# Optimization experiments

Hardware: AMD Instinct MI355X
Metric: run time of the kernel (lower is better)

Reference implementation:

```python
import jax, jax.numpy as jnp
import numpy as np

EMBED_DIM = 1024
NUM_HEADS = 16
B, L = 4, 2048


def setup_inputs() -> dict:
    key = jax.random.key(0)
    ks = jax.random.split(key, 5)
    scale = 0.02
    return {
        "x": jax.random.normal(ks[0], (B, L, EMBED_DIM), dtype=jnp.float32),
        "Wqkv_w": jax.random.normal(ks[1], (3 * EMBED_DIM, EMBED_DIM), dtype=jnp.float32) * scale,
        "Wqkv_b": jax.random.normal(ks[2], (3 * EMBED_DIM,), dtype=jnp.float32) * scale,
        "out_w": jax.random.normal(ks[3], (EMBED_DIM, EMBED_DIM), dtype=jnp.float32) * scale,
        "out_b": jax.random.normal(ks[4], (EMBED_DIM,), dtype=jnp.float32) * scale,
    }


def reference(x, Wqkv_w, Wqkv_b, out_w, out_b):
    Bb, Ll, D = x.shape
    H = NUM_HEADS
    hd = D // H
    # fused QKV projection (torch Linear: x @ W.T + b)
    qkv = jnp.einsum("bld,ed->ble", x, Wqkv_w) + Wqkv_b  # [B, L, 3D]
    q, k, v = jnp.split(qkv, 3, axis=-1)
    # [B, H, L, hd]
    q = q.reshape(Bb, Ll, H, hd).transpose(0, 2, 1, 3)
    k = k.reshape(Bb, Ll, H, hd).transpose(0, 2, 1, 3)
    v = v.reshape(Bb, Ll, H, hd).transpose(0, 2, 1, 3)
    scale = 1.0 / jnp.sqrt(jnp.asarray(hd, dtype=x.dtype))
    scores = jnp.einsum("bhqd,bhkd->bhqk", q, k) * scale  # [B, H, L, L]
    # causal mask (upper triangle above diagonal masked)
    causal = jnp.tril(jnp.ones((Ll, Ll), dtype=bool))
    scores = jnp.where(causal, scores, jnp.asarray(-jnp.inf, dtype=scores.dtype))
    attn = jax.nn.softmax(scores, axis=-1)
    attn_out = jnp.einsum("bhqk,bhkd->bhqd", attn, v)  # [B, H, L, hd]
    attn_out = attn_out.transpose(0, 2, 1, 3).reshape(Bb, Ll, D)
    out = jnp.einsum("bld,ed->ble", attn_out, out_w) + out_b
    return out
```

## Files before the change

kernel.cpp:

```cpp
#include <hip/hip_runtime.h>
#include <stdint.h>

#define DEV __device__ __forceinline__

typedef unsigned short u16;
typedef __bf16 bf16x8 __attribute__((ext_vector_type(8)));
typedef float f32x4 __attribute__((ext_vector_type(4)));
typedef u16 u16x8 __attribute__((ext_vector_type(8)));

#define MFMA_BF16(A, B, C) __builtin_amdgcn_mfma_f32_16x16x32_bf16(A, B, C, 0, 0, 0)
#define EXP2(x) __builtin_amdgcn_exp2f(x)

DEV u16 f2bf(float f) {
    unsigned x;
    __builtin_memcpy(&x, &f, 4);
    unsigned r = (x + 0x7fffu + ((x >> 16) & 1u)) >> 16;
    return (u16)r;
}

DEV u16 f2bf_fast(float f) {
    unsigned x;
    __builtin_memcpy(&x, &f, 4);
    return (u16)((x + 0x8000u) >> 16);
}

DEV void storeC(u16* p, float v) { *p = f2bf(v); }
DEV void storeC(float* p, float v) { *p = v; }

DEV void async_copy16(const u16* g, u16* l) {
    __builtin_amdgcn_global_load_lds(
        (__attribute__((address_space(1))) unsigned int*)g,
        (__attribute__((address_space(3))) unsigned int*)l, 16, 0, 0);
}

constexpr int N_X = 8192 * 1024, N_WQ = 3072 * 1024, N_WO = 1024 * 1024;

__global__ __launch_bounds__(256)
void cvt_all(const float* __restrict__ x, const float* __restrict__ wq,
             const float* __restrict__ wo, u16* __restrict__ out) {
    const int i = (blockIdx.x * 256 + threadIdx.x) * 4;
    const float* src;
    if (i < N_X) src = x + i;
    else if (i < N_X + N_WQ) src = wq + (i - N_X);
    else src = wo + (i - N_X - N_WQ);
    const float4 v = *(const float4*)src;
    ushort4 o;
    o.x = f2bf(v.x);
    o.y = f2bf(v.y);
    o.z = f2bf(v.z);
    o.w = f2bf(v.w);
    *(ushort4*)(out + i) = o;
}

template <typename OT, bool VSPLIT>
__global__ __launch_bounds__(256, 2)
void gemm_bt_bias(const u16* __restrict__ A, const u16* __restrict__ Bw,
                  const float* __restrict__ bias, OT* __restrict__ C,
                  u16* __restrict__ vT, int M, int N, int K) {
    __shared__ __attribute__((aligned(16))) u16 sA[2][128 * 32];
    __shared__ __attribute__((aligned(16))) u16 sB[2][128 * 32];

    const int tid  = threadIdx.x;
    const int lane = tid & 63;
    const int wave = tid >> 6;
    const int m0 = blockIdx.x * 128;
    const int n0 = blockIdx.y * 128;
    const int wm = (wave & 1) * 64;
    const int wn = (wave >> 1) * 64;
    const int fr = lane & 15;
    const int q4 = lane >> 4;

    const int r0 = tid >> 2;
    const int c0 = (tid & 3) * 8;
    const u16* gA0 = A + (size_t)(m0 + r0) * K + c0;
    const u16* gA1 = A + (size_t)(m0 + 64 + r0) * K + c0;
    const u16* gB0 = Bw + (size_t)(n0 + r0) * K + c0;
    const u16* gB1 = Bw + (size_t)(n0 + 64 + r0) * K + c0;

    f32x4 acc[4][4];
#pragma unroll
    for (int i = 0; i < 4; i++)
#pragma unroll
        for (int j = 0; j < 4; j++) acc[i][j] = (f32x4){0.f, 0.f, 0.f, 0.f};

    for (int k0 = 0; k0 < K; k0 += 64) {
#pragma unroll
        for (int p = 0; p < 2; ++p) {
            async_copy16(gA0 + k0 + p * 32, &sA[p][tid * 8]);
            async_copy16(gA1 + k0 + p * 32, &sA[p][2048 + tid * 8]);
            async_copy16(gB0 + k0 + p * 32, &sB[p][tid * 8]);
            async_copy16(gB1 + k0 + p * 32, &sB[p][2048 + tid * 8]);
        }
        __syncthreads();

#pragma unroll
        for (int p = 0; p < 2; ++p) {
            bf16x8 af[4], bfr[4];
#pragma unroll
            for (int i = 0; i < 4; i++)
                af[i] = *(const bf16x8*)&sA[p][(wm + i * 16 + fr) * 32 + q4 * 8];
#pragma unroll
            for (int j = 0; j < 4; j++)
                bfr[j] = *(const bf16x8*)&sB[p][(wn + j * 16 + fr) * 32 + q4 * 8];
#pragma unroll
            for (int i = 0; i < 4; i++)
#pragma unroll
                for (int j = 0; j < 4; j++)
                    acc[i][j] = MFMA_BF16(af[i], bfr[j], acc[i][j]);
        }
        __syncthreads();
    }

#pragma unroll
    for (int j = 0; j < 4; j++) {
        const int col = n0 + wn + j * 16 + fr;
        const float bv = bias[col];
        if (VSPLIT && col >= 2048) {
#pragma unroll
            for (int i = 0; i < 4; i++) {
                const int row = m0 + wm + i * 16 + q4 * 4;
                ushort4 o;
                o.x = f2bf(acc[i][j][0] + bv);
                o.y = f2bf(acc[i][j][1] + bv);
                o.z = f2bf(acc[i][j][2] + bv);
                o.w = f2bf(acc[i][j][3] + bv);
                *(ushort4*)&vT[(size_t)(col - 2048) * 8192 + row] = o;
            }
        } else {
#pragma unroll
            for (int i = 0; i < 4; i++) {
                const int row = m0 + wm + i * 16 + q4 * 4;
#pragma unroll
                for (int r = 0; r < 4; r++)
                    storeC(&C[(size_t)(row + r) * N + col], acc[i][j][r] + bv);
            }
        }
    }
}

constexpr int Lc = 2048, Dc = 1024;

__global__ __launch_bounds__(256, 4)
void attn_fa(const u16* __restrict__ qkv, const u16* __restrict__ vT,
             u16* __restrict__ outb) {
    __shared__ __attribute__((aligned(16))) u16 sK[64 * 72];
    __shared__ __attribute__((aligned(16))) u16 sVT[64 * 72];
    __shared__ __attribute__((aligned(16))) u16 sP[4][2][16 * 72];

    const int tid  = threadIdx.x;
    const int lane = tid & 63;
    const int wave = tid >> 6;
    const int fr = lane & 15;
    const int q4 = lane >> 4;

    const int id = blockIdx.x;
    const int g  = (id & 7) + 8 * (id >> 7);
    const int bx = (id >> 3) & 15;
    const int h = g & 15;
    const int b = g >> 4;
    const int qblkA = bx;
    const int qblkB = 31 - bx;

    constexpr float CEXP = 0.18033688011112042f;

    const int qrowA = qblkA * 64 + wave * 16 + fr;
    const int qrowB = qblkB * 64 + wave * 16 + fr;
    const u16* qptrA = qkv + ((size_t)(b * Lc + qrowA) * 3) * Dc + h * 64;
    const u16* qptrB = qkv + ((size_t)(b * Lc + qrowB) * 3) * Dc + h * 64;
    bf16x8 qfA[2], qfB[2];
    qfA[0] = *(const bf16x8*)(qptrA + q4 * 8);
    qfA[1] = *(const bf16x8*)(qptrA + 32 + q4 * 8);
    qfB[0] = *(const bf16x8*)(qptrB + q4 * 8);
    qfB[1] = *(const bf16x8*)(qptrB + 32 + q4 * 8);

    f32x4 oA[4], oB[4];
#pragma unroll
    for (int t = 0; t < 4; t++) {
        oA[t] = (f32x4){0.f, 0.f, 0.f, 0.f};
        oB[t] = (f32x4){0.f, 0.f, 0.f, 0.f};
    }
    float mA = -3.4e38f, lA = 0.f, mB = -3.4e38f, lB = 0.f;

    const int q_local = wave * 16 + fr;

    const int rr = tid >> 3;
    const int oo = tid & 7;
    const u16* kg = qkv + ((size_t)(b * Lc) * 3 + 1) * Dc + h * 64 + oo * 8;
    const u16* vg = vT + (size_t)(h * 64) * 8192 + b * Lc + oo * 8;

    u16x8 kr[2], vr[2];
#pragma unroll
    for (int c = 0; c < 2; ++c) {
        kr[c] = *(const u16x8*)(kg + (size_t)(c * 32 + rr) * 3072);
        vr[c] = *(const u16x8*)(vg + (size_t)(c * 32 + rr) * 8192);
    }

    u16* sPA = &sP[wave][0][0];
    u16* sPB = &sP[wave][1][0];

    for (int jb = 0; jb <= qblkB; ++jb) {
        __syncthreads();
#pragma unroll
        for (int c = 0; c < 2; ++c) {
            *(u16x8*)&sK[(c * 32 + rr) * 72 + oo * 8] = kr[c];
            *(u16x8*)&sVT[(c * 32 + rr) * 72 + oo * 8] = vr[c];
        }
        __syncthreads();
        if (jb < qblkB) {
#pragma unroll
            for (int c = 0; c < 2; ++c) {
                kr[c] = *(const u16x8*)(kg + (size_t)((jb + 1) * 64 + c * 32 + rr) * 3072);
                vr[c] = *(const u16x8*)(vg + (size_t)(c * 32 + rr) * 8192 + (jb + 1) * 64);
            }
        }

        const bool doA = (jb <= qblkA);

        f32x4 sA_[4], sB_[4];
#pragma unroll
        for (int t = 0; t < 4; t++) {
            const bf16x8 kf0 = *(const bf16x8*)&sK[(t * 16 + fr) * 72 + q4 * 8];
            const bf16x8 kf1 = *(const bf16x8*)&sK[(t * 16 + fr) * 72 + 32 + q4 * 8];
            sB_[t] = (f32x4){0.f, 0.f, 0.f, 0.f};
            sB_[t] = MFMA_BF16(kf0, qfB[0], sB_[t]);
            sB_[t] = MFMA_BF16(kf1, qfB[1], sB_[t]);
            if (doA) {
                sA_[t] = (f32x4){0.f, 0.f, 0.f, 0.f};
                sA_[t] = MFMA_BF16(kf0, qfA[0], sA_[t]);
                sA_[t] = MFMA_BF16(kf1, qfA[1], sA_[t]);
            }
        }

        {
            if (jb == qblkB) {
#pragma unroll
                for (int t = 0; t < 4; t++)
#pragma unroll
                    for (int r = 0; r < 4; r++)
                        if (t * 16 + q4 * 4 + r > q_local) sB_[t][r] = -1e30f;
            }
            float mx = sB_[0][0];
#pragma unroll
            for (int t = 0; t < 4; t++)
#pragma unroll
                for (int r = 0; r < 4; r++) mx = fmaxf(mx, sB_[t][r]);
            mx = fmaxf(mx, __shfl_xor(mx, 16));
            mx = fmaxf(mx, __shfl_xor(mx, 32));
            const float mnew = fmaxf(mB, mx);
            const float alpha = EXP2((mB - mnew) * CEXP);
            float sum = 0.f;
#pragma unroll
            for (int t = 0; t < 4; t++) {
#pragma unroll
                for (int r = 0; r < 4; r++) {
                    const float p = EXP2((sB_[t][r] - mnew) * CEXP);
                    sB_[t][r] = p;
                    sum += p;
                }
                ushort4 o;
                o.x = f2bf_fast(sB_[t][0]);
                o.y = f2bf_fast(sB_[t][1]);
                o.z = f2bf_fast(sB_[t][2]);
                o.w = f2bf_fast(sB_[t][3]);
                *(ushort4*)&sPB[fr * 72 + t * 16 + q4 * 4] = o;
            }
            sum += __shfl_xor(sum, 16);
            sum += __shfl_xor(sum, 32);
            lB = alpha * lB + sum;
            mB = mnew;
#pragma unroll
            for (int t = 0; t < 4; t++)
#pragma unroll
                for (int r = 0; r < 4; r++) oB[t][r] *= alpha;
        }

        if (doA) {
            if (jb == qblkA) {
#pragma unroll
                for (int t = 0; t < 4; t++)
#pragma unroll
                    for (int r = 0; r < 4; r++)
                        if (t * 16 + q4 * 4 + r > q_local) sA_[t][r] = -1e30f;
            }
            float mx = sA_[0][0];
#pragma unroll
            for (int t = 0; t < 4; t++)
#pragma unroll
                for (int r = 0; r < 4; r++) mx = fmaxf(mx, sA_[t][r]);
            mx = fmaxf(mx, __shfl_xor(mx, 16));
            mx = fmaxf(mx, __shfl_xor(mx, 32));
            const float mnew = fmaxf(mA, mx);
            const float alpha = EXP2((mA - mnew) * CEXP);
            float sum = 0.f;
#pragma unroll
            for (int t = 0; t < 4; t++) {
#pragma unroll
                for (int r = 0; r < 4; r++) {
                    const float p = EXP2((sA_[t][r] - mnew) * CEXP);
                    sA_[t][r] = p;
                    sum += p;
                }
                ushort4 o;
                o.x = f2bf_fast(sA_[t][0]);
                o.y = f2bf_fast(sA_[t][1]);
                o.z = f2bf_fast(sA_[t][2]);
                o.w = f2bf_fast(sA_[t][3]);
                *(ushort4*)&sPA[fr * 72 + t * 16 + q4 * 4] = o;
            }
            sum += __shfl_xor(sum, 16);
            sum += __shfl_xor(sum, 32);
            lA = alpha * lA + sum;
            mA = mnew;
#pragma unroll
            for (int t = 0; t < 4; t++)
#pragma unroll
                for (int r = 0; r < 4; r++) oA[t][r] *= alpha;
        }

#pragma unroll
        for (int ks = 0; ks < 2; ++ks) {
            const bf16x8 pfB = *(const bf16x8*)&sPB[fr * 72 + ks * 32 + q4 * 8];
            bf16x8 pfA;
            if (doA) pfA = *(const bf16x8*)&sPA[fr * 72 + ks * 32 + q4 * 8];
#pragma unroll
            for (int t = 0; t < 4; t++) {
                const bf16x8 vf = *(const bf16x8*)&sVT[(t * 16 + fr) * 72 + ks * 32 + q4 * 8];
                oB[t] = MFMA_BF16(vf, pfB, oB[t]);
                if (doA) oA[t] = MFMA_BF16(vf, pfA, oA[t]);
            }
        }
    }

    const float rlA = 1.0f / lA;
    const float rlB = 1.0f / lB;
    u16* orowA = outb + (size_t)(b * Lc + qblkA * 64 + wave * 16 + fr) * Dc + h * 64;
    u16* orowB = outb + (size_t)(b * Lc + qblkB * 64 + wave * 16 + fr) * Dc + h * 64;
#pragma unroll
    for (int t = 0; t < 4; t++) {
        ushort4 a, o;
        a.x = f2bf(oA[t][0] * rlA);
        a.y = f2bf(oA[t][1] * rlA);
        a.z = f2bf(oA[t][2] * rlA);
        a.w = f2bf(oA[t][3] * rlA);
        *(ushort4*)(orowA + t * 16 + q4 * 4) = a;
        o.x = f2bf(oB[t][0] * rlB);
        o.y = f2bf(oB[t][1] * rlB);
        o.z = f2bf(oB[t][2] * rlB);
        o.w = f2bf(oB[t][3] * rlB);
        *(ushort4*)(orowB + t * 16 + q4 * 4) = o;
    }
}

extern "C" void kernel_launch(void* const* d_in, const int* in_sizes, int n_in,
                              void* d_out, int out_size, void* d_ws, size_t ws_size,
                              hipStream_t stream) {
    const float* x    = (const float*)d_in[0];
    const float* wqkv = (const float*)d_in[1];
    const float* bqkv = (const float*)d_in[2];
    const float* wout = (const float*)d_in[3];
    const float* bout = (const float*)d_in[4];
    float* out = (float*)d_out;

    u16* qkv    = (u16*)d_ws;
    u16* attn   = qkv + (size_t)8192 * 3072;
    u16* xbf    = attn + (size_t)8192 * 1024;
    u16* wqkvbf = xbf + (size_t)8192 * 1024;
    u16* woutbf = wqkvbf + (size_t)3072 * 1024;
    u16* vT     = woutbf + (size_t)1024 * 1024;

    dim3 blk(256);
    cvt_all<<<(N_X + N_WQ + N_WO) / 1024, blk, 0, stream>>>(x, wqkv, wout, xbf);

    gemm_bt_bias<u16, true><<<dim3(8192 / 128, 3072 / 128), blk, 0, stream>>>(
        xbf, wqkvbf, bqkv, qkv, vT, 8192, 3072, 1024);
    attn_fa<<<dim3(1024), blk, 0, stream>>>(qkv, vT, attn);
    gemm_bt_bias<float, false><<<dim3(8192 / 128, 1024 / 128), blk, 0, stream>>>(
        attn, woutbf, bout, out, nullptr, 8192, 1024, 1024);
}
```

Measured before the change: 267.1 us.

## Rewrite GEMMs with 8-wave 256x128 tiles, triple-buffered LDS, and swizzled layout

Replaces the 4-wave 128x128 double-sync GEMM with a 512-thread kernel computing 256x128 tiles using a 3-stage LDS ring of 64-wide K slices, XOR-swizzled shared memory, and prefetch loads interleaved between two MFMA phases with s_setprio. Also remaps block IDs across XCDs for L2 locality. The aim is to hide global-load latency behind MFMA work and cut LDS bank conflicts. In exchange it uses far more LDS per block (144KB), which limits occupancy, and adds more barriers per K step.

```diff
diff --git a/kernel.cpp b/kernel.cpp
--- a/kernel.cpp
+++ b/kernel.cpp
@@ -31,6 +31,12 @@
     __builtin_amdgcn_global_load_lds(
         (__attribute__((address_space(1))) unsigned int*)g,
         (__attribute__((address_space(3))) unsigned int*)l, 16, 0, 0);
+}
+
+DEV void wg_barrier() {
+    asm volatile("" ::: "memory");
+    __builtin_amdgcn_s_barrier();
+    asm volatile("" ::: "memory");
 }
 
 constexpr int N_X = 8192 * 1024, N_WQ = 3072 * 1024, N_WO = 1024 * 1024;
@@ -53,29 +59,33 @@
 }
 
 template <typename OT, bool VSPLIT>
-__global__ __launch_bounds__(256, 2)
-void gemm_bt_bias(const u16* __restrict__ A, const u16* __restrict__ Bw,
-                  const float* __restrict__ bias, OT* __restrict__ C,
-                  u16* __restrict__ vT, int M, int N, int K) {
-    __shared__ __attribute__((aligned(16))) u16 sA[2][128 * 32];
-    __shared__ __attribute__((aligned(16))) u16 sB[2][128 * 32];
+__global__ __launch_bounds__(512, 2)
+void gemm_8ph(const u16* __restrict__ A, const u16* __restrict__ Bw,
+              const float* __restrict__ bias, OT* __restrict__ C,
+              u16* __restrict__ vT, int M, int N, int K, int ntn) {
+    __shared__ __attribute__((aligned(16))) u16 sA[3][256 * 64];
+    __shared__ __attribute__((aligned(16))) u16 sB[3][128 * 64];
 
     const int tid  = threadIdx.x;
     const int lane = tid & 63;
     const int wave = tid >> 6;
-    const int m0 = blockIdx.x * 128;
-    const int n0 = blockIdx.y * 128;
-    const int wm = (wave & 1) * 64;
-    const int wn = (wave >> 1) * 64;
     const int fr = lane & 15;
     const int q4 = lane >> 4;
-
-    const int r0 = tid >> 2;
-    const int c0 = (tid & 3) * 8;
-    const u16* gA0 = A + (size_t)(m0 + r0) * K + c0;
-    const u16* gA1 = A + (size_t)(m0 + 64 + r0) * K + c0;
-    const u16* gB0 = Bw + (size_t)(n0 + r0) * K + c0;
-    const u16* gB1 = Bw + (size_t)(n0 + 64 + r0) * K + c0;
+    const int wr = wave >> 1;
+    const int wc = wave & 1;
+
+    const int cpx = gridDim.x >> 3;
+    const int wg = (blockIdx.x & 7) * cpx + (blockIdx.x >> 3);
+    const int mt = wg / ntn, nt = wg % ntn;
+    const int m0 = mt * 256, n0 = nt * 128;
+
+    const int crow = tid >> 3;
+    const int ccol = ((tid & 7) ^ (crow & 7)) * 8;
+    const u16* pA = A + (size_t)(m0 + crow) * K + ccol;
+    const u16* pB = Bw + (size_t)(n0 + crow) * K + ccol;
+    const size_t rK = (size_t)64 * K;
+
+    const int NT = K >> 6;
 
     f32x4 acc[4][4];
 #pragma unroll
@@ -83,42 +93,99 @@
 #pragma unroll
         for (int j = 0; j < 4; j++) acc[i][j] = (f32x4){0.f, 0.f, 0.f, 0.f};
 
-    for (int k0 = 0; k0 < K; k0 += 64) {
-#pragma unroll
-        for (int p = 0; p < 2; ++p) {
-            async_copy16(gA0 + k0 + p * 32, &sA[p][tid * 8]);
-            async_copy16(gA1 + k0 + p * 32, &sA[p][2048 + tid * 8]);
-            async_copy16(gB0 + k0 + p * 32, &sB[p][tid * 8]);
-            async_copy16(gB1 + k0 + p * 32, &sB[p][2048 + tid * 8]);
-        }
-        __syncthreads();
-
-#pragma unroll
-        for (int p = 0; p < 2; ++p) {
-            bf16x8 af[4], bfr[4];
-#pragma unroll
-            for (int i = 0; i < 4; i++)
-                af[i] = *(const bf16x8*)&sA[p][(wm + i * 16 + fr) * 32 + q4 * 8];
-#pragma unroll
-            for (int j = 0; j < 4; j++)
-                bfr[j] = *(const bf16x8*)&sB[p][(wn + j * 16 + fr) * 32 + q4 * 8];
-#pragma unroll
-            for (int i = 0; i < 4; i++)
-#pragma unroll
-                for (int j = 0; j < 4; j++)
-                    acc[i][j] = MFMA_BF16(af[i], bfr[j], acc[i][j]);
-        }
-        __syncthreads();
+#pragma unroll
+    for (int p = 0; p < 4; p++) async_copy16(pA + p * rK, &sA[0][p * 4096 + tid * 8]);
+#pragma unroll
+    for (int p = 0; p < 2; p++) async_copy16(pB + p * rK, &sB[0][p * 4096 + tid * 8]);
+#pragma unroll
+    for (int p = 0; p < 4; p++) async_copy16(pA + p * rK + 64, &sA[1][p * 4096 + tid * 8]);
+#pragma unroll
+    for (int p = 0; p < 2; p++) async_copy16(pB + p * rK + 64, &sB[1][p * 4096 + tid * 8]);
+    asm volatile("s_waitcnt vmcnt(6)" ::: "memory");
+    wg_barrier();
+
+    int sl = 0;
+    for (int t = 0; t < NT; ++t) {
+        const u16* bufA = sA[sl];
+        const u16* bufB = sB[sl];
+        const int s2 = (sl >= 1) ? sl - 1 : 2;
+        const bool st = (t + 2 < NT);
+        const int ko = (t + 2) * 64;
+
+        bf16x8 af[4][2], bf[4][2];
+
+#pragma unroll
+        for (int i = 0; i < 4; i++) {
+            const int row = wr * 64 + i * 16 + fr;
+#pragma unroll
+            for (int kk = 0; kk < 2; kk++)
+                af[i][kk] = *(const bf16x8*)
+                    &bufA[row * 64 + (((kk * 64 + q4 * 16) ^ ((row & 7) << 4)) >> 1)];
+        }
+#pragma unroll
+        for (int j = 0; j < 2; j++) {
+            const int row = wc * 64 + j * 16 + fr;
+#pragma unroll
+            for (int kk = 0; kk < 2; kk++)
+                bf[j][kk] = *(const bf16x8*)
+                    &bufB[row * 64 + (((kk * 64 + q4 * 16) ^ ((row & 7) << 4)) >> 1)];
+        }
+        if (st) {
+#pragma unroll
+            for (int p = 0; p < 3; p++)
+                async_copy16(pA + p * rK + ko, &sA[s2][p * 4096 + tid * 8]);
+        }
+        wg_barrier();
+        __builtin_amdgcn_s_setprio(1);
+#pragma unroll
+        for (int i = 0; i < 4; i++)
+#pragma unroll
+            for (int j = 0; j < 2; j++) {
+                acc[i][j] = MFMA_BF16(af[i][0], bf[j][0], acc[i][j]);
+                acc[i][j] = MFMA_BF16(af[i][1], bf[j][1], acc[i][j]);
+            }
+        __builtin_amdgcn_s_setprio(0);
+        wg_barrier();
+
+#pragma unroll
+        for (int j = 2; j < 4; j++) {
+            const int row = wc * 64 + j * 16 + fr;
+#pragma unroll
+            for (int kk = 0; kk < 2; kk++)
+                bf[j][kk] = *(const bf16x8*)
+                    &bufB[row * 64 + (((kk * 64 + q4 * 16) ^ ((row & 7) << 4)) >> 1)];
+        }
+        if (st) {
+            async_copy16(pA + 3 * rK + ko, &sA[s2][3 * 4096 + tid * 8]);
+#pragma unroll
+            for (int p = 0; p < 2; p++)
+                async_copy16(pB + p * rK + ko, &sB[s2][p * 4096 + tid * 8]);
+        }
+        if (t < NT - 2) asm volatile("s_waitcnt vmcnt(6)" ::: "memory");
+        else            asm volatile("s_waitcnt vmcnt(0)" ::: "memory");
+        wg_barrier();
+        __builtin_amdgcn_s_setprio(1);
+#pragma unroll
+        for (int i = 0; i < 4; i++)
+#pragma unroll
+            for (int j = 2; j < 4; j++) {
+                acc[i][j] = MFMA_BF16(af[i][0], bf[j][0], acc[i][j]);
+                acc[i][j] = MFMA_BF16(af[i][1], bf[j][1], acc[i][j]);
+            }
+        __builtin_amdgcn_s_setprio(0);
+        wg_barrier();
+
+        sl = (sl < 2) ? sl + 1 : 0;
     }
 
 #pragma unroll
     for (int j = 0; j < 4; j++) {
-        const int col = n0 + wn + j * 16 + fr;
+        const int col = n0 + wc * 64 + j * 16 + fr;
         const float bv = bias[col];
         if (VSPLIT && col >= 2048) {
 #pragma unroll
             for (int i = 0; i < 4; i++) {
-                const int row = m0 + wm + i * 16 + q4 * 4;
+                const int row = m0 + wr * 64 + i * 16 + q4 * 4;
                 ushort4 o;
                 o.x = f2bf(acc[i][j][0] + bv);
                 o.y = f2bf(acc[i][j][1] + bv);
@@ -129,7 +196,7 @@
         } else {
 #pragma unroll
             for (int i = 0; i < 4; i++) {
-                const int row = m0 + wm + i * 16 + q4 * 4;
+                const int row = m0 + wr * 64 + i * 16 + q4 * 4;
 #pragma unroll
                 for (int r = 0; r < 4; r++)
                     storeC(&C[(size_t)(row + r) * N + col], acc[i][j][r] + bv);
@@ -368,12 +435,11 @@
     u16* woutbf = wqkvbf + (size_t)3072 * 1024;
     u16* vT     = woutbf + (size_t)1024 * 1024;
 
-    dim3 blk(256);
-    cvt_all<<<(N_X + N_WQ + N_WO) / 1024, blk, 0, stream>>>(x, wqkv, wout, xbf);
-
-    gemm_bt_bias<u16, true><<<dim3(8192 / 128, 3072 / 128), blk, 0, stream>>>(
-        xbf, wqkvbf, bqkv, qkv, vT, 8192, 3072, 1024);
-    attn_fa<<<dim3(1024), blk, 0, stream>>>(qkv, vT, attn);
-    gemm_bt_bias<float, false><<<dim3(8192 / 128, 1024 / 128), blk, 0, stream>>>(
-        attn, woutbf, bout, out, nullptr, 8192, 1024, 1024);
-}
+    cvt_all<<<(N_X + N_WQ + N_WO) / 1024, dim3(256), 0, stream>>>(x, wqkv, wout, xbf);
+
+    gemm_8ph<u16, true><<<dim3(768), dim3(512), 0, stream>>>(
+        xbf, wqkvbf, bqkv, qkv, vT, 8192, 3072, 1024, 24);
+    attn_fa<<<dim3(1024), dim3(256), 0, stream>>>(qkv, vT, attn);
+    gemm_8ph<float, false><<<dim3(256), dim3(512), 0, stream>>>(
+        attn, woutbf, bout, out, nullptr, 8192, 1024, 1024, 8);
+}
```

Result: no change. 267.9 us (+0.3%).

## Process four query blocks per attention workgroup to reuse K/V tiles

Applied to the files above, without the earlier changes.

Each attention workgroup now handles four causally balanced query blocks (bx, 15-bx, 16+bx, 31-bx) instead of two, so every K/V tile staged in shared memory serves up to four query blocks. The grid is halved to 512 workgroups and launch bounds drop to 2 waves-per-EU to make room for the larger register state (four O accumulators and four Q fragments). This reduces global K/V loads and barrier count per unit of work, but it lowers occupancy and parallelism: with 512 workgroups on a 256-CU part there may be under-filled CUs and less latency hiding.

```diff
diff --git a/kernel.cpp b/kernel.cpp
--- a/kernel.cpp
+++ b/kernel.cpp
@@ -140,12 +140,12 @@
 
 constexpr int Lc = 2048, Dc = 1024;
 
-__global__ __launch_bounds__(256, 4)
+__global__ __launch_bounds__(256, 2)
 void attn_fa(const u16* __restrict__ qkv, const u16* __restrict__ vT,
              u16* __restrict__ outb) {
     __shared__ __attribute__((aligned(16))) u16 sK[64 * 72];
     __shared__ __attribute__((aligned(16))) u16 sVT[64 * 72];
-    __shared__ __attribute__((aligned(16))) u16 sP[4][2][16 * 72];
+    __shared__ __attribute__((aligned(16))) u16 sP[4][4][16 * 72];
 
     const int tid  = threadIdx.x;
     const int lane = tid & 63;
@@ -154,32 +154,35 @@
     const int q4 = lane >> 4;
 
     const int id = blockIdx.x;
-    const int g  = (id & 7) + 8 * (id >> 7);
-    const int bx = (id >> 3) & 15;
+    const int g  = (id & 7) + 8 * (id >> 6);
+    const int bx = (id >> 3) & 7;
     const int h = g & 15;
     const int b = g >> 4;
-    const int qblkA = bx;
-    const int qblkB = 31 - bx;
+    const int qA = bx, qB = 15 - bx, qC = 16 + bx, qD = 31 - bx;
 
     constexpr float CEXP = 0.18033688011112042f;
 
-    const int qrowA = qblkA * 64 + wave * 16 + fr;
-    const int qrowB = qblkB * 64 + wave * 16 + fr;
-    const u16* qptrA = qkv + ((size_t)(b * Lc + qrowA) * 3) * Dc + h * 64;
-    const u16* qptrB = qkv + ((size_t)(b * Lc + qrowB) * 3) * Dc + h * 64;
-    bf16x8 qfA[2], qfB[2];
-    qfA[0] = *(const bf16x8*)(qptrA + q4 * 8);
-    qfA[1] = *(const bf16x8*)(qptrA + 32 + q4 * 8);
-    qfB[0] = *(const bf16x8*)(qptrB + q4 * 8);
-    qfB[1] = *(const bf16x8*)(qptrB + 32 + q4 * 8);
-
-    f32x4 oA[4], oB[4];
+    bf16x8 qfA[2], qfB[2], qfC[2], qfD[2];
+#define LOADQ(qf, qblk)                                                     \
+    {                                                                       \
+        const int qrow = (qblk) * 64 + wave * 16 + fr;                      \
+        const u16* qp = qkv + ((size_t)(b * Lc + qrow) * 3) * Dc + h * 64;  \
+        qf[0] = *(const bf16x8*)(qp + q4 * 8);                              \
+        qf[1] = *(const bf16x8*)(qp + 32 + q4 * 8);                         \
+    }
+    LOADQ(qfA, qA) LOADQ(qfB, qB) LOADQ(qfC, qC) LOADQ(qfD, qD)
+#undef LOADQ
+
+    f32x4 oA[4], oB[4], oC[4], oD[4];
 #pragma unroll
     for (int t = 0; t < 4; t++) {
         oA[t] = (f32x4){0.f, 0.f, 0.f, 0.f};
         oB[t] = (f32x4){0.f, 0.f, 0.f, 0.f};
+        oC[t] = (f32x4){0.f, 0.f, 0.f, 0.f};
+        oD[t] = (f32x4){0.f, 0.f, 0.f, 0.f};
     }
     float mA = -3.4e38f, lA = 0.f, mB = -3.4e38f, lB = 0.f;
+    float mC = -3.4e38f, lC = 0.f, mD = -3.4e38f, lD = 0.f;
 
     const int q_local = wave * 16 + fr;
 
@@ -197,8 +200,48 @@
 
     u16* sPA = &sP[wave][0][0];
     u16* sPB = &sP[wave][1][0];
-
-    for (int jb = 0; jb <= qblkB; ++jb) {
+    u16* sPC = &sP[wave][2][0];
+    u16* sPD = &sP[wave][3][0];
+
+#define SM_TILE(S, mS, lS, oS, sPp, qblk)                                   \
+    {                                                                       \
+        if (jb == (qblk)) {                                                 \
+            _Pragma("unroll") for (int t = 0; t < 4; t++)                   \
+                _Pragma("unroll") for (int r = 0; r < 4; r++)               \
+                    if (t * 16 + q4 * 4 + r > q_local) S[t][r] = -1e30f;    \
+        }                                                                   \
+        float mx = S[0][0];                                                 \
+        _Pragma("unroll") for (int t = 0; t < 4; t++)                       \
+            _Pragma("unroll") for (int r = 0; r < 4; r++)                   \
+                mx = fmaxf(mx, S[t][r]);                                    \
+        mx = fmaxf(mx, __shfl_xor(mx, 16));                                 \
+        mx = fmaxf(mx, __shfl_xor(mx, 32));                                 \
+        const float mnew = fmaxf(mS, mx);                                   \
+        const float alpha = EXP2((mS - mnew) * CEXP);                       \
+        float sum = 0.f;                                                    \
+        _Pragma("unroll") for (int t = 0; t < 4; t++) {                     \
+            _Pragma("unroll") for (int r = 0; r < 4; r++) {                 \
+                const float p = EXP2((S[t][r] - mnew) * CEXP);              \
+                S[t][r] = p;                                                \
+                sum += p;                                                   \
+            }                                                               \
+            ushort4 o;                                                      \
+            o.x = f2bf_fast(S[t][0]);                                       \
+            o.y = f2bf_fast(S[t][1]);                                       \
+            o.z = f2bf_fast(S[t][2]);                                       \
+            o.w = f2bf_fast(S[t][3]);                                       \
+            *(ushort4*)&sPp[fr * 72 + t * 16 + q4 * 4] = o;                 \
+        }                                                                   \
+        sum += __shfl_xor(sum, 16);                                         \
+        sum += __shfl_xor(sum, 32);                                         \
+        lS = alpha * lS + sum;                                              \
+        mS = mnew;                                                          \
+        _Pragma("unroll") for (int t = 0; t < 4; t++)                       \
+            _Pragma("unroll") for (int r = 0; r < 4; r++)                   \
+                oS[t][r] *= alpha;                                          \
+    }
+
+    for (int jb = 0; jb <= qD; ++jb) {
         __syncthreads();
 #pragma unroll
         for (int c = 0; c < 2; ++c) {
@@ -206,7 +249,7 @@
             *(u16x8*)&sVT[(c * 32 + rr) * 72 + oo * 8] = vr[c];
         }
         __syncthreads();
-        if (jb < qblkB) {
+        if (jb < qD) {
 #pragma unroll
             for (int c = 0; c < 2; ++c) {
                 kr[c] = *(const u16x8*)(kg + (size_t)((jb + 1) * 64 + c * 32 + rr) * 3072);
@@ -214,16 +257,28 @@
             }
         }
 
-        const bool doA = (jb <= qblkA);
-
-        f32x4 sA_[4], sB_[4];
+        const bool doA = (jb <= qA);
+        const bool doB = (jb <= qB);
+        const bool doC = (jb <= qC);
+
+        f32x4 sA_[4], sB_[4], sC_[4], sD_[4];
 #pragma unroll
         for (int t = 0; t < 4; t++) {
             const bf16x8 kf0 = *(const bf16x8*)&sK[(t * 16 + fr) * 72 + q4 * 8];
             const bf16x8 kf1 = *(const bf16x8*)&sK[(t * 16 + fr) * 72 + 32 + q4 * 8];
-            sB_[t] = (f32x4){0.f, 0.f, 0.f, 0.f};
-            sB_[t] = MFMA_BF16(kf0, qfB[0], sB_[t]);
-            sB_[t] = MFMA_BF16(kf1, qfB[1], sB_[t]);
+            sD_[t] = (f32x4){0.f, 0.f, 0.f, 0.f};
+            sD_[t] = MFMA_BF16(kf0, qfD[0], sD_[t]);
+            sD_[t] = MFMA_BF16(kf1, qfD[1], sD_[t]);
+            if (doC) {
+                sC_[t] = (f32x4){0.f, 0.f, 0.f, 0.f};
+                sC_[t] = MFMA_BF16(kf0, qfC[0], sC_[t]);
+                sC_[t] = MFMA_BF16(kf1, qfC[1], sC_[t]);
+            }
+            if (doB) {
+                sB_[t] = (f32x4){0.f, 0.f, 0.f, 0.f};
+                sB_[t] = MFMA_BF16(kf0, qfB[0], sB_[t]);
+                sB_[t] = MFMA_BF16(kf1, qfB[1], sB_[t]);
+            }
             if (doA) {
                 sA_[t] = (f32x4){0.f, 0.f, 0.f, 0.f};
                 sA_[t] = MFMA_BF16(kf0, qfA[0], sA_[t]);
@@ -231,124 +286,49 @@
             }
         }
 
-        {
-            if (jb == qblkB) {
-#pragma unroll
-                for (int t = 0; t < 4; t++)
-#pragma unroll
-                    for (int r = 0; r < 4; r++)
-                        if (t * 16 + q4 * 4 + r > q_local) sB_[t][r] = -1e30f;
-            }
-            float mx = sB_[0][0];
-#pragma unroll
-            for (int t = 0; t < 4; t++)
-#pragma unroll
-                for (int r = 0; r < 4; r++) mx = fmaxf(mx, sB_[t][r]);
-            mx = fmaxf(mx, __shfl_xor(mx, 16));
-            mx = fmaxf(mx, __shfl_xor(mx, 32));
-            const float mnew = fmaxf(mB, mx);
-            const float alpha = EXP2((mB - mnew) * CEXP);
-            float sum = 0.f;
-#pragma unroll
-            for (int t = 0; t < 4; t++) {
-#pragma unroll
-                for (int r = 0; r < 4; r++) {
-                    const float p = EXP2((sB_[t][r] - mnew) * CEXP);
-                    sB_[t][r] = p;
-                    sum += p;
-                }
-                ushort4 o;
-                o.x = f2bf_fast(sB_[t][0]);
-                o.y = f2bf_fast(sB_[t][1]);
-                o.z = f2bf_fast(sB_[t][2]);
-                o.w = f2bf_fast(sB_[t][3]);
-                *(ushort4*)&sPB[fr * 72 + t * 16 + q4 * 4] = o;
-            }
-            sum += __shfl_xor(sum, 16);
-            sum += __shfl_xor(sum, 32);
-            lB = alpha * lB + sum;
-            mB = mnew;
-#pragma unroll
-            for (int t = 0; t < 4; t++)
-#pragma unroll
-                for (int r = 0; r < 4; r++) oB[t][r] *= alpha;
-        }
-
-        if (doA) {
-            if (jb == qblkA) {
-#pragma unroll
-                for (int t = 0; t < 4; t++)
-#pragma unroll
-                    for (int r = 0; r < 4; r++)
-                        if (t * 16 + q4 * 4 + r > q_local) sA_[t][r] = -1e30f;
-            }
-            float mx = sA_[0][0];
-#pragma unroll
-            for (int t = 0; t < 4; t++)
-#pragma unroll
-                for (int r = 0; r < 4; r++) mx = fmaxf(mx, sA_[t][r]);
-            mx = fmaxf(mx, __shfl_xor(mx, 16));
-            mx = fmaxf(mx, __shfl_xor(mx, 32));
-            const float mnew = fmaxf(mA, mx);
-            const float alpha = EXP2((mA - mnew) * CEXP);
-            float sum = 0.f;
-#pragma unroll
-            for (int t = 0; t < 4; t++) {
-#pragma unroll
-                for (int r = 0; r < 4; r++) {
-                    const float p = EXP2((sA_[t][r] - mnew) * CEXP);
-                    sA_[t][r] = p;
-                    sum += p;
-                }
-                ushort4 o;
-                o.x = f2bf_fast(sA_[t][0]);
-                o.y = f2bf_fast(sA_[t][1]);
-                o.z = f2bf_fast(sA_[t][2]);
-                o.w = f2bf_fast(sA_[t][3]);
-                *(ushort4*)&sPA[fr * 72 + t * 16 + q4 * 4] = o;
-            }
-            sum += __shfl_xor(sum, 16);
-            sum += __shfl_xor(sum, 32);
-            lA = alpha * lA + sum;
-            mA = mnew;
-#pragma unroll
-            for (int t = 0; t < 4; t++)
-#pragma unroll
-                for (int r = 0; r < 4; r++) oA[t][r] *= alpha;
-        }
+        SM_TILE(sD_, mD, lD, oD, sPD, qD);
+        if (doC) SM_TILE(sC_, mC, lC, oC, sPC, qC);
+        if (doB) SM_TILE(sB_, mB, lB, oB, sPB, qB);
+        if (doA) SM_TILE(sA_, mA, lA, oA, sPA, qA);
 
 #pragma unroll
         for (int ks = 0; ks < 2; ++ks) {
-            const bf16x8 pfB = *(const bf16x8*)&sPB[fr * 72 + ks * 32 + q4 * 8];
-            bf16x8 pfA;
+            const bf16x8 pfD = *(const bf16x8*)&sPD[fr * 72 + ks * 32 + q4 * 8];
+            bf16x8 pfC, pfB, pfA;
+            if (doC) pfC = *(const bf16x8*)&sPC[fr * 72 + ks * 32 + q4 * 8];
+            if (doB) pfB = *(const bf16x8*)&sPB[fr * 72 + ks * 32 + q4 * 8];
             if (doA) pfA = *(const bf16x8*)&sPA[fr * 72 + ks * 32 + q4 * 8];
 #pragma unroll
             for (int t = 0; t < 4; t++) {
                 const bf16x8 vf = *(const bf16x8*)&sVT[(t * 16 + fr) * 72 + ks * 32 + q4 * 8];
-                oB[t] = MFMA_BF16(vf, pfB, oB[t]);
+                oD[t] = MFMA_BF16(vf, pfD, oD[t]);
+                if (doC) oC[t] = MFMA_BF16(vf, pfC, oC[t]);
+                if (doB) oB[t] = MFMA_BF16(vf, pfB, oB[t]);
                 if (doA) oA[t] = MFMA_BF16(vf, pfA, oA[t]);
             }
         }
     }
-
-    const float rlA = 1.0f / lA;
-    const float rlB = 1.0f / lB;
-    u16* orowA = outb + (size_t)(b * Lc + qblkA * 64 + wave * 16 + fr) * Dc + h * 64;
-    u16* orowB = outb + (size_t)(b * Lc + qblkB * 64 + wave * 16 + fr) * Dc + h * 64;
-#pragma unroll
-    for (int t = 0; t < 4; t++) {
-        ushort4 a, o;
-        a.x = f2bf(oA[t][0] * rlA);
-        a.y = f2bf(oA[t][1] * rlA);
-        a.z = f2bf(oA[t][2] * rlA);
-        a.w = f2bf(oA[t][3] * rlA);
-        *(ushort4*)(orowA + t * 16 + q4 * 4) = a;
-        o.x = f2bf(oB[t][0] * rlB);
-        o.y = f2bf(oB[t][1] * rlB);
-        o.z = f2bf(oB[t][2] * rlB);
-        o.w = f2bf(oB[t][3] * rlB);
-        *(ushort4*)(orowB + t * 16 + q4 * 4) = o;
-    }
+#undef SM_TILE
+
+#define WR_OUT(oS, lS, qblk)                                                      \
+    {                                                                             \
+        const float rl = 1.0f / lS;                                               \
+        u16* orow =                                                               \
+            outb + (size_t)(b * Lc + (qblk) * 64 + wave * 16 + fr) * Dc + h * 64; \
+        _Pragma("unroll") for (int t = 0; t < 4; t++) {                           \
+            ushort4 o;                                                            \
+            o.x = f2bf(oS[t][0] * rl);                                            \
+            o.y = f2bf(oS[t][1] * rl);                                            \
+            o.z = f2bf(oS[t][2] * rl);                                            \
+            o.w = f2bf(oS[t][3] * rl);                                            \
+            *(ushort4*)(orow + t * 16 + q4 * 4) = o;                              \
+        }                                                                         \
+    }
+    WR_OUT(oA, lA, qA)
+    WR_OUT(oB, lB, qB)
+    WR_OUT(oC, lC, qC)
+    WR_OUT(oD, lD, qD)
+#undef WR_OUT
 }
 
 extern "C" void kernel_launch(void* const* d_in, const int* in_sizes, int n_in,
@@ -373,7 +353,7 @@
 
     gemm_bt_bias<u16, true><<<dim3(8192 / 128, 3072 / 128), blk, 0, stream>>>(
         xbf, wqkvbf, bqkv, qkv, vT, 8192, 3072, 1024);
-    attn_fa<<<dim3(1024), blk, 0, stream>>>(qkv, vT, attn);
+    attn_fa<<<dim3(512), blk, 0, stream>>>(qkv, vT, attn);
     gemm_bt_bias<float, false><<<dim3(8192 / 128, 1024 / 128), blk, 0, stream>>>(
         attn, woutbf, bout, out, nullptr, 8192, 1024, 1024);
 }
```

After: 270.7 us. No clear change (+1.3%).
